# Kernel tuning notes

Hardware: AMD Instinct MI355X
Metric: run time of the kernel (lower is better)

The kernel has to match this reference:

```python
import jax, jax.numpy as jnp
import numpy as np

B, S, D = 2, 2048, 2048
H, KVH, HD = 8, 1, 256          # query heads, kv heads, head_dim (GQA: n_rep = H // KVH)
ROPE_THETA = 10000.0
NEG_INF = -1e9


def setup_inputs() -> dict:
    key = jax.random.key(0)
    k1, k2, k3, k4, k5 = jax.random.split(key, 5)
    hidden_states = jax.random.normal(k1, (B, S, D), dtype=jnp.float32)
    # additive causal mask: 0 where allowed, -inf where masked, shape (B,1,S,S)
    causal = jnp.tril(jnp.ones((S, S), dtype=bool))
    attention_mask = jnp.where(causal, 0.0, NEG_INF).astype(jnp.float32)
    attention_mask = jnp.broadcast_to(attention_mask[None, None], (B, 1, S, S))
    position_ids = jnp.broadcast_to(jnp.arange(S, dtype=jnp.int32)[None, :], (B, S))
    sc = 0.02
    Wq = jax.random.normal(k2, (H * HD, D), dtype=jnp.float32) * sc   # torch Linear weight layout [out,in]
    Wk = jax.random.normal(k3, (KVH * HD, D), dtype=jnp.float32) * sc
    Wv = jax.random.normal(k4, (KVH * HD, D), dtype=jnp.float32) * sc
    Wo = jax.random.normal(k5, (D, H * HD), dtype=jnp.float32) * sc
    return {"hidden_states": hidden_states, "attention_mask": attention_mask,
            "position_ids": position_ids, "Wq": Wq, "Wk": Wk, "Wv": Wv, "Wo": Wo}


def _rotate_half(x):
    x1, x2 = jnp.split(x, 2, axis=-1)
    return jnp.concatenate((-x2, x1), axis=-1)


def _rope_cos_sin(position_ids):
    inv_freq = 1.0 / (ROPE_THETA ** (jnp.arange(0, HD, 2, dtype=jnp.float32) / HD))  # [HD/2]
    freqs = position_ids.astype(jnp.float32)[:, :, None] * inv_freq[None, None, :]   # [B,S,HD/2]
    emb = jnp.concatenate((freqs, freqs), axis=-1)                                   # [B,S,HD]
    return jnp.cos(emb)[:, None], jnp.sin(emb)[:, None]                              # [B,1,S,HD]


def reference(hidden_states, attention_mask, position_ids, Wq, Wk, Wv, Wo):
    q = (hidden_states @ Wq.T).reshape(B, S, H, HD).transpose(0, 2, 1, 3)     # [B,H,S,HD]
    k = (hidden_states @ Wk.T).reshape(B, S, KVH, HD).transpose(0, 2, 1, 3)   # [B,KVH,S,HD]
    v = (hidden_states @ Wv.T).reshape(B, S, KVH, HD).transpose(0, 2, 1, 3)
    cos, sin = _rope_cos_sin(position_ids)
    q = q * cos + _rotate_half(q) * sin
    k = k * cos + _rotate_half(k) * sin
    n_rep = H // KVH
    k = jnp.repeat(k, n_rep, axis=1)                                          # repeat_kv -> [B,H,S,HD]
    v = jnp.repeat(v, n_rep, axis=1)
    scores = jnp.einsum('bhqd,bhkd->bhqk', q, k) / jnp.sqrt(jnp.float32(HD))
    scores = scores + attention_mask
    attn = jax.nn.softmax(scores, axis=-1)                                    # dropout p=0 (eval)
    ctx = jnp.einsum('bhqk,bhkd->bhqd', attn, v)
    ctx = ctx.transpose(0, 2, 1, 3).reshape(B, S, H * HD)
    out = ctx @ Wo.T
    return out, attn
```

## Files before the change

### kernel.cpp

```cpp
#include <hip/hip_runtime.h>
#include <hip/hip_bf16.h>
#include <math.h>

typedef __bf16 bf16_t;
typedef __bf16 bf16x8 __attribute__((ext_vector_type(8)));
typedef float  f32x4  __attribute__((ext_vector_type(4)));

#define DEV __device__ __forceinline__

constexpr int B_   = 2;
constexpr int S_   = 2048;
constexpr int D_   = 2048;
constexpr int H_   = 8;
constexpr int HD_  = 256;
constexpr int NQKV_ = H_ * HD_ + 2 * HD_;
constexpr int TOK_ = B_ * S_;
constexpr int CHK_ = 64 * HD_;

#if defined(__has_builtin)
#if __has_builtin(__builtin_amdgcn_global_load_lds)
#define HAS_GLLDS 1
#endif
#endif

DEV void stage16(const bf16_t* g, bf16_t* l) {
#ifdef HAS_GLLDS
  __builtin_amdgcn_global_load_lds((const __attribute__((address_space(1))) void*)g,
                                   (__attribute__((address_space(3))) void*)l, 16, 0, 0);
#else
  *(bf16x8*)l = *(const bf16x8*)g;
#endif
}

__global__ void cast_inputs(const float* __restrict__ hs, const float* __restrict__ wq,
                            const float* __restrict__ wk, const float* __restrict__ wv,
                            const float* __restrict__ wo,
                            bf16_t* __restrict__ Xb, bf16_t* __restrict__ Wqkvb,
                            bf16_t* __restrict__ Wob) {
  const size_t i = (size_t)blockIdx.x * blockDim.x + threadIdx.x;
  const size_t NHS = (size_t)TOK_ * D_;
  const size_t NWQ = (size_t)H_ * HD_ * D_;
  const size_t NWK = (size_t)HD_ * D_;
  if (i < NHS) Xb[i] = (bf16_t)hs[i];
  if (i < NWQ) { Wqkvb[i] = (bf16_t)wq[i]; Wob[i] = (bf16_t)wo[i]; }
  if (i < NWK) { Wqkvb[NWQ + i] = (bf16_t)wk[i]; Wqkvb[NWQ + NWK + i] = (bf16_t)wv[i]; }
}

DEV void tile_k64_db(const bf16_t* __restrict__ Ab, const bf16_t* __restrict__ Bg,
                     int K, int lda, int ldb, int m0, int n0,
                     bf16_t* Asm, bf16_t* Bsm,
                     f32x4 acc[4][4],
                     int tid, int lrow, int quad, int wm, int wn)
{
  const int sw = (lrow & 1) << 2;
  int srow[4], sg[4];
  #pragma unroll
  for (int c = 0; c < 4; ++c) {
    int chunk = c * 256 + tid;
    srow[c] = chunk >> 3;
    sg[c]   = (chunk & 7) ^ ((srow[c] & 1) << 2);
  }
  #pragma unroll
  for (int c = 0; c < 4; ++c) {
    int chunk = c * 256 + tid;
    stage16(Ab + (size_t)(m0 + srow[c]) * lda + sg[c] * 8, &Asm[chunk * 8]);
    stage16(Bg + (size_t)(n0 + srow[c]) * ldb + sg[c] * 8, &Bsm[chunk * 8]);
  }
  const int nT = K >> 6;
  for (int t = 0; t < nT; ++t) {
    const int cur = (t & 1) * (128 * 64);
    const int nxt = ((t + 1) & 1) * (128 * 64);
    __syncthreads();
    if (t + 1 < nT) {
      const int k0 = (t + 1) << 6;
      #pragma unroll
      for (int c = 0; c < 4; ++c) {
        int chunk = c * 256 + tid;
        stage16(Ab + (size_t)(m0 + srow[c]) * lda + (k0 + sg[c] * 8), &Asm[nxt + chunk * 8]);
        stage16(Bg + (size_t)(n0 + srow[c]) * ldb + (k0 + sg[c] * 8), &Bsm[nxt + chunk * 8]);
      }
    }
    #pragma unroll
    for (int kk = 0; kk < 2; ++kk) {
      bf16x8 af[4], bfr[4];
      #pragma unroll
      for (int i = 0; i < 4; ++i)
        af[i] = *(const bf16x8*)&Asm[cur + (wm + i * 16 + lrow) * 64 + ((quad + kk * 4) ^ sw) * 8];
      #pragma unroll
      for (int j = 0; j < 4; ++j)
        bfr[j] = *(const bf16x8*)&Bsm[cur + (wn + j * 16 + lrow) * 64 + ((quad + kk * 4) ^ sw) * 8];
      #pragma unroll
      for (int i = 0; i < 4; ++i)
        #pragma unroll
        for (int j = 0; j < 4; ++j)
          acc[i][j] = __builtin_amdgcn_mfma_f32_16x16x32_bf16(af[i], bfr[j], acc[i][j], 0, 0, 0);
    }
  }
}

template <bool CBF16>
__global__ __launch_bounds__(256, 2)
void gemm_bt(const bf16_t* __restrict__ Ab, const bf16_t* __restrict__ Bg,
             void* __restrict__ Cv, int K, int lda, int ldb, int ldc)
{
  const int nwg = gridDim.x * gridDim.y;
  const int w0  = blockIdx.y * gridDim.x + blockIdx.x;
  const int q   = nwg >> 3;
  const int logical = (w0 & 7) * q + (w0 >> 3);
  const int bm = logical / gridDim.x, bn = logical % gridDim.x;
  const int m0 = bm * 128, n0 = bn * 128;

  __shared__ __align__(16) bf16_t Asm[2 * 128 * 64];
  __shared__ __align__(16) bf16_t Bsm[2 * 128 * 64];

  const int tid  = threadIdx.x;
  const int l    = tid & 63;
  const int w    = tid >> 6;
  const int wm   = (w >> 1) * 64;
  const int wn   = (w & 1) * 64;
  const int lrow = l & 15;
  const int quad = l >> 4;

  f32x4 acc[4][4] = {};
  tile_k64_db(Ab, Bg, K, lda, ldb, m0, n0, Asm, Bsm, acc, tid, lrow, quad, wm, wn);

  #pragma unroll
  for (int i = 0; i < 4; ++i) {
    int row = wm + i * 16 + quad * 4;
    #pragma unroll
    for (int j = 0; j < 4; ++j) {
      int col = n0 + wn + j * 16 + lrow;
      #pragma unroll
      for (int r = 0; r < 4; ++r) {
        if (CBF16) ((bf16_t*)Cv)[(size_t)(m0 + row + r) * ldc + col] = (bf16_t)acc[i][j][r];
        else       ((float*) Cv)[(size_t)(m0 + row + r) * ldc + col] = acc[i][j][r];
      }
    }
  }
}

__global__ void rope_kernel(const bf16_t* __restrict__ qkv, const int* __restrict__ pos_ids,
                            bf16_t* __restrict__ Qh, bf16_t* __restrict__ Kb,
                            bf16_t* __restrict__ K2)
{
  const int t = blockIdx.x;
  const int b = t >> 11, s = t & (S_ - 1);
  const int tid = threadIdx.x;
  const int h = tid >> 5, c = tid & 31;
  const float pos = (float)pos_ids[t];
  const int pdbase = (c & 15) * 8;
  float cs[8], sn[8];
  #pragma unroll
  for (int j = 0; j < 8; ++j) {
    float invf = exp2f((float)(pdbase + j) * -0.103810253f);
    float ang = pos * invf;
    cs[j] = cosf(ang); sn[j] = sinf(ang);
  }
  const float sgn = (c < 16) ? -1.0f : 1.0f;
  const bf16_t* base = qkv + (size_t)t * NQKV_;

  {
    bf16x8 x  = *(const bf16x8*)(base + h * HD_ + c * 8);
    bf16x8 xo = *(const bf16x8*)(base + h * HD_ + (c ^ 16) * 8);
    bf16x8 o;
    #pragma unroll
    for (int j = 0; j < 8; ++j)
      o[j] = (bf16_t)((float)x[j] * cs[j] + sgn * (float)xo[j] * sn[j]);
    *(bf16x8*)(Qh + ((size_t)(b * H_ + h) * S_ + s) * HD_ + c * 8) = o;
  }
  if (h == 0) {
    bf16x8 x  = *(const bf16x8*)(base + D_ + c * 8);
    bf16x8 xo = *(const bf16x8*)(base + D_ + (c ^ 16) * 8);
    bf16x8 o;
    #pragma unroll
    for (int j = 0; j < 8; ++j)
      o[j] = (bf16_t)((float)x[j] * cs[j] + sgn * (float)xo[j] * sn[j]);
    *(bf16x8*)(Kb + (size_t)t * HD_ + c * 8) = o;
    const int chunk = s >> 6, key = s & 63;
    *(bf16x8*)(K2 + (size_t)(b * 32 + chunk) * CHK_ + c * 512 + key * 8) = o;
  }
}

__global__ void v_trans(const bf16_t* __restrict__ qkv, bf16_t* __restrict__ V2)
{
  const int blk = blockIdx.x;
  const int s0 = (blk & 31) * 64;
  const int b = blk >> 5;
  const int tid = threadIdx.x;
  __shared__ bf16_t L[64][264];
  #pragma unroll
  for (int it = 0; it < 8; ++it) {
    int gi = it * 256 + tid;
    int r = gi >> 5, cc = gi & 31;
    *(bf16x8*)&L[r][cc * 8] =
        *(const bf16x8*)(qkv + ((size_t)b * S_ + s0 + r) * NQKV_ + (D_ + HD_) + cc * 8);
  }
  __syncthreads();
  bf16_t* out = V2 + (size_t)blk * CHK_;
  #pragma unroll
  for (int it = 0; it < 8; ++it) {
    int G = it * 256 + tid;
    bf16x8 o;
    #pragma unroll
    for (int j = 0; j < 8; ++j) o[j] = L[it * 8 + j][tid];
    *(bf16x8*)(out + (size_t)G * 8) = o;
  }
}

constexpr int PSTR = 136;

DEV void compute_S(const bf16_t* __restrict__ K2g, bf16_t* __restrict__ KV,
                   const bf16x8 aq[8], f32x4 accS[8],
                   int kb, int tid, int lrow, int quad)
{
  #pragma unroll
  for (int half = 0; half < 2; ++half) {
    __syncthreads();
    const bf16_t* src = K2g + (size_t)(kb * 2 + half) * CHK_;
    #pragma unroll
    for (int it = 0; it < 8; ++it) {
      int s = it * 256 + tid;
      stage16(src + (size_t)s * 8, KV + s * 8);
    }
    __syncthreads();
    __builtin_amdgcn_s_setprio(1);
    #pragma unroll
    for (int kk = 0; kk < 8; ++kk) {
      bf16x8 bk[4];
      #pragma unroll
      for (int j = 0; j < 4; ++j)
        bk[j] = *(const bf16x8*)&KV[((kk * 4 + quad) * 64 + j * 16 + lrow) * 8];
      #pragma unroll
      for (int j = 0; j < 4; ++j)
        accS[half * 4 + j] =
            __builtin_amdgcn_mfma_f32_16x16x32_bf16(aq[kk], bk[j], accS[half * 4 + j], 0, 0, 0);
    }
    __builtin_amdgcn_s_setprio(0);
  }
}

__global__ __launch_bounds__(256, 2)
void flash_attn(const bf16_t* __restrict__ Qh, const bf16_t* __restrict__ K2,
                const bf16_t* __restrict__ V2, bf16_t* __restrict__ Ctx,
                float* __restrict__ lsum)
{
  const int idx = blockIdx.x;
  int z, qb;
  if (idx < 256) { z = idx & 15; qb = idx >> 4; }
  else           { int j = idx - 256; z = j & 15; qb = 31 - (j >> 4); }
  const int b = z >> 3, h = z & 7;
  const int q0 = qb * 64;
  const bf16_t* Qg  = Qh + ((size_t)z * S_ + q0) * HD_;
  const bf16_t* K2g = K2 + (size_t)b * 32 * CHK_;
  const bf16_t* V2g = V2 + (size_t)b * 32 * CHK_;

  __shared__ __align__(16) bf16_t KV[64 * 256];
  __shared__ __align__(16) bf16_t Pst[4 * 16 * PSTR];

  const int tid = threadIdx.x;
  const int w = tid >> 6, l = tid & 63;
  const int lrow = l & 15, quad = l >> 4;
  const int nkb = (qb >> 1) + 1;
  const float scale = 0.0625f;

  bf16x8 aq[8];
  const bf16_t* qrow = Qg + (size_t)(w * 16 + lrow) * HD_ + quad * 8;
  #pragma unroll
  for (int kk = 0; kk < 8; ++kk) aq[kk] = *(const bf16x8*)(qrow + kk * 32);

  const int rowg0 = q0 + w * 16 + quad * 4;
  float lp[4] = {0.f, 0.f, 0.f, 0.f};
  f32x4 accO[16] = {};
  bf16_t* pw = &Pst[w * 16 * PSTR];

  for (int kb = 0; kb < nkb; ++kb) {
    f32x4 accS[8] = {};
    compute_S(K2g, KV, aq, accS, kb, tid, lrow, quad);
    __syncthreads();

    {
      const bf16_t* src = V2g + (size_t)(kb * 2 + 0) * CHK_;
      #pragma unroll
      for (int it = 0; it < 8; ++it) {
        int s = it * 256 + tid;
        stage16(src + (size_t)s * 8, KV + s * 8);
      }
    }

    #pragma unroll
    for (int r = 0; r < 4; ++r) {
      #pragma unroll
      for (int j = 0; j < 8; ++j) {
        int col = kb * 128 + j * 16 + lrow;
        float p = (col <= rowg0 + r) ? __expf(accS[j][r] * scale) : 0.f;
        lp[r] += p;
        pw[(quad * 4 + r) * PSTR + j * 16 + lrow] = (bf16_t)p;
      }
    }
    bf16x8 ap[4];
    #pragma unroll
    for (int kk2 = 0; kk2 < 4; ++kk2)
      ap[kk2] = *(const bf16x8*)&pw[lrow * PSTR + kk2 * 32 + quad * 8];

    __syncthreads();
    __builtin_amdgcn_s_setprio(1);
    #pragma unroll
    for (int kkl = 0; kkl < 2; ++kkl) {
      #pragma unroll
      for (int j2 = 0; j2 < 16; ++j2) {
        bf16x8 bv = *(const bf16x8*)&KV[((kkl * 4 + quad) * 256 + j2 * 16 + lrow) * 8];
        accO[j2] = __builtin_amdgcn_mfma_f32_16x16x32_bf16(ap[kkl], bv, accO[j2], 0, 0, 0);
      }
    }
    __builtin_amdgcn_s_setprio(0);

    __syncthreads();
    {
      const bf16_t* src = V2g + (size_t)(kb * 2 + 1) * CHK_;
      #pragma unroll
      for (int it = 0; it < 8; ++it) {
        int s = it * 256 + tid;
        stage16(src + (size_t)s * 8, KV + s * 8);
      }
    }
    __syncthreads();
    __builtin_amdgcn_s_setprio(1);
    #pragma unroll
    for (int kkl = 0; kkl < 2; ++kkl) {
      #pragma unroll
      for (int j2 = 0; j2 < 16; ++j2) {
        bf16x8 bv = *(const bf16x8*)&KV[((kkl * 4 + quad) * 256 + j2 * 16 + lrow) * 8];
        accO[j2] = __builtin_amdgcn_mfma_f32_16x16x32_bf16(ap[2 + kkl], bv, accO[j2], 0, 0, 0);
      }
    }
    __builtin_amdgcn_s_setprio(0);
  }

  #pragma unroll
  for (int r = 0; r < 4; ++r) {
    #pragma unroll
    for (int o = 1; o < 16; o <<= 1) lp[r] += __shfl_xor(lp[r], o, 64);
  }
  float inv[4];
  #pragma unroll
  for (int r = 0; r < 4; ++r) inv[r] = 1.0f / lp[r];

  #pragma unroll
  for (int j2 = 0; j2 < 16; ++j2) {
    #pragma unroll
    for (int r = 0; r < 4; ++r) {
      int rowq = q0 + w * 16 + quad * 4 + r;
      Ctx[((size_t)b * S_ + rowq) * D_ + h * HD_ + j2 * 16 + lrow] = (bf16_t)(accO[j2][r] * inv[r]);
    }
  }
  if (lrow == 0) {
    #pragma unroll
    for (int r = 0; r < 4; ++r) lsum[(size_t)z * S_ + rowg0 + r] = lp[r];
  }
}

__global__ __launch_bounds__(256, 2)
void p_writer(const bf16_t* __restrict__ Qh, const bf16_t* __restrict__ Kbp,
              const float* __restrict__ lsum, float* __restrict__ attn)
{
  const int w0 = (blockIdx.z * gridDim.y + blockIdx.y) * gridDim.x + blockIdx.x;
  const int logical = (w0 & 7) * 512 + (w0 >> 3);
  const int z = logical >> 8, bm = (logical >> 4) & 15, bn = logical & 15;
  const int m0 = bm * 128, n0 = bn * 128;
  float* Pg = attn + (size_t)z * S_ * S_;
  const int tid = threadIdx.x;

  if (bn > bm) {
    #pragma unroll
    for (int it = 0; it < 16; ++it) {
      int idx = it * 256 + tid;
      int row = idx >> 5, c4 = idx & 31;
      *(f32x4*)&Pg[(size_t)(m0 + row) * S_ + n0 + c4 * 4] = f32x4{0.f, 0.f, 0.f, 0.f};
    }
    return;
  }

  const bf16_t* Ab = Qh + (size_t)z * S_ * HD_;
  const bf16_t* Bg = Kbp + (size_t)(z >> 3) * S_ * HD_;

  __shared__ __align__(16) bf16_t Asm[2 * 128 * 64];
  __shared__ __align__(16) bf16_t Bsm[2 * 128 * 64];

  const int l    = tid & 63;
  const int w    = tid >> 6;
  const int wm   = (w >> 1) * 64;
  const int wn   = (w & 1) * 64;
  const int lrow = l & 15;
  const int quad = l >> 4;

  f32x4 acc[4][4] = {};
  tile_k64_db(Ab, Bg, HD_, HD_, HD_, m0, n0, Asm, Bsm, acc, tid, lrow, quad, wm, wn);

  const float scale = 0.0625f;
  #pragma unroll
  for (int i = 0; i < 4; ++i) {
    int row = m0 + wm + i * 16 + quad * 4;
    #pragma unroll
    for (int r = 0; r < 4; ++r) {
      const float il = 1.0f / lsum[(size_t)z * S_ + row + r];
      float* prow = &Pg[(size_t)(row + r) * S_];
      #pragma unroll
      for (int j = 0; j < 4; ++j) {
        int col = n0 + wn + j * 16 + lrow;
        prow[col] = (col <= row + r) ? __expf(acc[i][j][r] * scale) * il : 0.f;
      }
    }
  }
}

extern "C" void kernel_launch(void* const* d_in, const int* in_sizes, int n_in,
                              void* d_out, int out_size, void* d_ws, size_t ws_size,
                              hipStream_t stream)
{
  const float* hs  = (const float*)d_in[0];
  const int*   pos = (const int*)d_in[2];
  const float* wq  = (const float*)d_in[3];
  const float* wk  = (const float*)d_in[4];
  const float* wv  = (const float*)d_in[5];
  const float* wo  = (const float*)d_in[6];

  float* out  = (float*)d_out;
  float* attn = out + (size_t)TOK_ * D_;

  char* ws = (char*)d_ws;
  bf16_t* Xb    = (bf16_t*)(ws);
  bf16_t* Wqkvb = (bf16_t*)(ws + 16777216);
  bf16_t* Wob   = (bf16_t*)(ws + 27262976);
  bf16_t* QKVb  = (bf16_t*)(ws + 35651584);
  bf16_t* Qh    = (bf16_t*)(ws + 56623104);
  bf16_t* Kb    = (bf16_t*)(ws + 73400320);
  bf16_t* V2    = (bf16_t*)(ws + 75497472);
  bf16_t* Ctx   = (bf16_t*)(ws + 77594624);
  float*  lsum  = (float* )(ws + 94371840);
  bf16_t* K2    = (bf16_t*)(ws + 94502912);

  cast_inputs<<<(TOK_ * D_) / 256, 256, 0, stream>>>(hs, wq, wk, wv, wo, Xb, Wqkvb, Wob);
  gemm_bt<true><<<dim3(NQKV_ / 128, TOK_ / 128), 256, 0, stream>>>(
      Xb, Wqkvb, QKVb, D_, D_, D_, NQKV_);
  rope_kernel<<<TOK_, 256, 0, stream>>>(QKVb, pos, Qh, Kb, K2);
  v_trans<<<B_ * 32, 256, 0, stream>>>(QKVb, V2);
  flash_attn<<<512, 256, 0, stream>>>(Qh, K2, V2, Ctx, lsum);
  p_writer<<<dim3(S_ / 128, S_ / 128, B_ * H_), 256, 0, stream>>>(Qh, Kb, lsum, attn);
  gemm_bt<false><<<dim3(D_ / 128, TOK_ / 128), 256, 0, stream>>>(
      Ctx, Wob, out, D_, D_, D_, D_);
}
```

Baseline: 616.1 us.

## Vectorize input cast and shrink GEMM K-tile to 32 without LDS swizzle

The fp32-to-bf16 cast kernel now processes four elements per thread with vector loads and stores, and launches a quarter as many blocks. The shared GEMM tile helper used by the projection GEMMs and the attention-probability writer drops from a K-step of 64 to 32. This halves LDS usage per block, which could allow more resident blocks, but doubles the number of barrier-separated iterations. The XOR swizzle on LDS columns is also removed, which risks bank conflicts on the fragment reads.

Measured after the change: 595.0 us. -3.4%, faster.

```diff
diff --git a/kernel.cpp b/kernel.cpp
--- a/kernel.cpp
+++ b/kernel.cpp
@@ -3,6 +3,7 @@
 #include <math.h>
 
 typedef __bf16 bf16_t;
+typedef __bf16 bf16x4 __attribute__((ext_vector_type(4)));
 typedef __bf16 bf16x8 __attribute__((ext_vector_type(8)));
 typedef float  f32x4  __attribute__((ext_vector_type(4)));
 
@@ -37,64 +38,78 @@
                             const float* __restrict__ wo,
                             bf16_t* __restrict__ Xb, bf16_t* __restrict__ Wqkvb,
                             bf16_t* __restrict__ Wob) {
-  const size_t i = (size_t)blockIdx.x * blockDim.x + threadIdx.x;
+  const size_t i4 = ((size_t)blockIdx.x * blockDim.x + threadIdx.x) * 4;
   const size_t NHS = (size_t)TOK_ * D_;
   const size_t NWQ = (size_t)H_ * HD_ * D_;
   const size_t NWK = (size_t)HD_ * D_;
-  if (i < NHS) Xb[i] = (bf16_t)hs[i];
-  if (i < NWQ) { Wqkvb[i] = (bf16_t)wq[i]; Wob[i] = (bf16_t)wo[i]; }
-  if (i < NWK) { Wqkvb[NWQ + i] = (bf16_t)wk[i]; Wqkvb[NWQ + NWK + i] = (bf16_t)wv[i]; }
-}
-
-DEV void tile_k64_db(const bf16_t* __restrict__ Ab, const bf16_t* __restrict__ Bg,
+  if (i4 < NHS) {
+    f32x4 v = *(const f32x4*)(hs + i4);
+    bf16x4 o; o[0]=(bf16_t)v[0]; o[1]=(bf16_t)v[1]; o[2]=(bf16_t)v[2]; o[3]=(bf16_t)v[3];
+    *(bf16x4*)(Xb + i4) = o;
+  }
+  if (i4 < NWQ) {
+    f32x4 v = *(const f32x4*)(wq + i4);
+    bf16x4 o; o[0]=(bf16_t)v[0]; o[1]=(bf16_t)v[1]; o[2]=(bf16_t)v[2]; o[3]=(bf16_t)v[3];
+    *(bf16x4*)(Wqkvb + i4) = o;
+    f32x4 v2 = *(const f32x4*)(wo + i4);
+    bf16x4 o2; o2[0]=(bf16_t)v2[0]; o2[1]=(bf16_t)v2[1]; o2[2]=(bf16_t)v2[2]; o2[3]=(bf16_t)v2[3];
+    *(bf16x4*)(Wob + i4) = o2;
+  }
+  if (i4 < NWK) {
+    f32x4 v = *(const f32x4*)(wk + i4);
+    bf16x4 o; o[0]=(bf16_t)v[0]; o[1]=(bf16_t)v[1]; o[2]=(bf16_t)v[2]; o[3]=(bf16_t)v[3];
+    *(bf16x4*)(Wqkvb + NWQ + i4) = o;
+    f32x4 v2 = *(const f32x4*)(wv + i4);
+    bf16x4 o2; o2[0]=(bf16_t)v2[0]; o2[1]=(bf16_t)v2[1]; o2[2]=(bf16_t)v2[2]; o2[3]=(bf16_t)v2[3];
+    *(bf16x4*)(Wqkvb + NWQ + NWK + i4) = o2;
+  }
+}
+
+DEV void tile_k32_db(const bf16_t* __restrict__ Ab, const bf16_t* __restrict__ Bg,
                      int K, int lda, int ldb, int m0, int n0,
                      bf16_t* Asm, bf16_t* Bsm,
                      f32x4 acc[4][4],
                      int tid, int lrow, int quad, int wm, int wn)
 {
-  const int sw = (lrow & 1) << 2;
-  int srow[4], sg[4];
-  #pragma unroll
-  for (int c = 0; c < 4; ++c) {
+  int srow[2], scol[2];
+  #pragma unroll
+  for (int c = 0; c < 2; ++c) {
     int chunk = c * 256 + tid;
-    srow[c] = chunk >> 3;
-    sg[c]   = (chunk & 7) ^ ((srow[c] & 1) << 2);
-  }
-  #pragma unroll
-  for (int c = 0; c < 4; ++c) {
+    srow[c] = chunk >> 2;
+    scol[c] = (chunk & 3) << 3;
+  }
+  #pragma unroll
+  for (int c = 0; c < 2; ++c) {
     int chunk = c * 256 + tid;
-    stage16(Ab + (size_t)(m0 + srow[c]) * lda + sg[c] * 8, &Asm[chunk * 8]);
-    stage16(Bg + (size_t)(n0 + srow[c]) * ldb + sg[c] * 8, &Bsm[chunk * 8]);
-  }
-  const int nT = K >> 6;
+    stage16(Ab + (size_t)(m0 + srow[c]) * lda + scol[c], &Asm[chunk * 8]);
+    stage16(Bg + (size_t)(n0 + srow[c]) * ldb + scol[c], &Bsm[chunk * 8]);
+  }
+  const int nT = K >> 5;
   for (int t = 0; t < nT; ++t) {
-    const int cur = (t & 1) * (128 * 64);
-    const int nxt = ((t + 1) & 1) * (128 * 64);
+    const int cur = (t & 1) * (128 * 32);
+    const int nxt = ((t + 1) & 1) * (128 * 32);
     __syncthreads();
     if (t + 1 < nT) {
-      const int k0 = (t + 1) << 6;
-      #pragma unroll
-      for (int c = 0; c < 4; ++c) {
+      const int k0 = (t + 1) << 5;
+      #pragma unroll
+      for (int c = 0; c < 2; ++c) {
         int chunk = c * 256 + tid;
-        stage16(Ab + (size_t)(m0 + srow[c]) * lda + (k0 + sg[c] * 8), &Asm[nxt + chunk * 8]);
-        stage16(Bg + (size_t)(n0 + srow[c]) * ldb + (k0 + sg[c] * 8), &Bsm[nxt + chunk * 8]);
-      }
-    }
-    #pragma unroll
-    for (int kk = 0; kk < 2; ++kk) {
-      bf16x8 af[4], bfr[4];
-      #pragma unroll
-      for (int i = 0; i < 4; ++i)
-        af[i] = *(const bf16x8*)&Asm[cur + (wm + i * 16 + lrow) * 64 + ((quad + kk * 4) ^ sw) * 8];
+        stage16(Ab + (size_t)(m0 + srow[c]) * lda + (k0 + scol[c]), &Asm[nxt + chunk * 8]);
+        stage16(Bg + (size_t)(n0 + srow[c]) * ldb + (k0 + scol[c]), &Bsm[nxt + chunk * 8]);
+      }
+    }
+    bf16x8 af[4], bfr[4];
+    #pragma unroll
+    for (int i = 0; i < 4; ++i)
+      af[i] = *(const bf16x8*)&Asm[cur + (wm + i * 16 + lrow) * 32 + quad * 8];
+    #pragma unroll
+    for (int j = 0; j < 4; ++j)
+      bfr[j] = *(const bf16x8*)&Bsm[cur + (wn + j * 16 + lrow) * 32 + quad * 8];
+    #pragma unroll
+    for (int i = 0; i < 4; ++i)
       #pragma unroll
       for (int j = 0; j < 4; ++j)
-        bfr[j] = *(const bf16x8*)&Bsm[cur + (wn + j * 16 + lrow) * 64 + ((quad + kk * 4) ^ sw) * 8];
-      #pragma unroll
-      for (int i = 0; i < 4; ++i)
-        #pragma unroll
-        for (int j = 0; j < 4; ++j)
-          acc[i][j] = __builtin_amdgcn_mfma_f32_16x16x32_bf16(af[i], bfr[j], acc[i][j], 0, 0, 0);
-    }
+        acc[i][j] = __builtin_amdgcn_mfma_f32_16x16x32_bf16(af[i], bfr[j], acc[i][j], 0, 0, 0);
   }
 }
 
@@ -110,8 +125,8 @@
   const int bm = logical / gridDim.x, bn = logical % gridDim.x;
   const int m0 = bm * 128, n0 = bn * 128;
 
-  __shared__ __align__(16) bf16_t Asm[2 * 128 * 64];
-  __shared__ __align__(16) bf16_t Bsm[2 * 128 * 64];
+  __shared__ __align__(16) bf16_t Asm[2 * 128 * 32];
+  __shared__ __align__(16) bf16_t Bsm[2 * 128 * 32];
 
   const int tid  = threadIdx.x;
   const int l    = tid & 63;
@@ -122,7 +137,7 @@
   const int quad = l >> 4;
 
   f32x4 acc[4][4] = {};
-  tile_k64_db(Ab, Bg, K, lda, ldb, m0, n0, Asm, Bsm, acc, tid, lrow, quad, wm, wn);
+  tile_k32_db(Ab, Bg, K, lda, ldb, m0, n0, Asm, Bsm, acc, tid, lrow, quad, wm, wn);
 
   #pragma unroll
   for (int i = 0; i < 4; ++i) {
@@ -383,8 +398,8 @@
   const bf16_t* Ab = Qh + (size_t)z * S_ * HD_;
   const bf16_t* Bg = Kbp + (size_t)(z >> 3) * S_ * HD_;
 
-  __shared__ __align__(16) bf16_t Asm[2 * 128 * 64];
-  __shared__ __align__(16) bf16_t Bsm[2 * 128 * 64];
+  __shared__ __align__(16) bf16_t Asm[2 * 128 * 32];
+  __shared__ __align__(16) bf16_t Bsm[2 * 128 * 32];
 
   const int l    = tid & 63;
   const int w    = tid >> 6;
@@ -394,7 +409,7 @@
   const int quad = l >> 4;
 
   f32x4 acc[4][4] = {};
-  tile_k64_db(Ab, Bg, HD_, HD_, HD_, m0, n0, Asm, Bsm, acc, tid, lrow, quad, wm, wn);
+  tile_k32_db(Ab, Bg, HD_, HD_, HD_, m0, n0, Asm, Bsm, acc, tid, lrow, quad, wm, wn);
 
   const float scale = 0.0625f;
   #pragma unroll
@@ -439,7 +454,7 @@
   float*  lsum  = (float* )(ws + 94371840);
   bf16_t* K2    = (bf16_t*)(ws + 94502912);
 
-  cast_inputs<<<(TOK_ * D_) / 256, 256, 0, stream>>>(hs, wq, wk, wv, wo, Xb, Wqkvb, Wob);
+  cast_inputs<<<(TOK_ * D_) / 1024, 256, 0, stream>>>(hs, wq, wk, wv, wo, Xb, Wqkvb, Wob);
   gemm_bt<true><<<dim3(NQKV_ / 128, TOK_ / 128), 256, 0, stream>>>(
       Xb, Wqkvb, QKVb, D_, D_, D_, NQKV_);
   rope_kernel<<<TOK_, 256, 0, stream>>>(QKVb, pos, Qh, Kb, K2);
```
